# Optimization experiments

Measured on AMD Instinct MI355X. Metric: run time of the kernel, lower is better.

## Reference

```python
import jax, jax.numpy as jnp
import numpy as np

HEADS = 16
DIM_HEAD = 64
SCALE = DIM_HEAD ** -0.5

def setup_inputs() -> dict:
    key = jax.random.key(0)
    k1, k2, k3 = jax.random.split(key, 3)
    dim = HEADS * DIM_HEAD  # 1024
    x = jax.random.normal(k1, (2, 4096, dim), dtype=jnp.float32)
    w_qkv = jax.random.normal(k2, (dim, 3 * dim), dtype=jnp.float32) * (dim ** -0.5)
    w_out = jax.random.normal(k3, (dim, dim), dtype=jnp.float32) * (dim ** -0.5)
    return {"x": x, "w_qkv": w_qkv, "w_out": w_out}

def reference(x, w_qkv, w_out):
    b, n, dim = x.shape
    qkv = x @ w_qkv  # (b, n, 3*h*d)
    qkv = qkv.reshape(b, n, 3, HEADS, DIM_HEAD)
    q, k, v = (qkv[:, :, 0], qkv[:, :, 1], qkv[:, :, 2])  # (b, n, h, d)
    q = jnp.swapaxes(q, 1, 2) * SCALE  # (b, h, n, d)
    k = jnp.swapaxes(k, 1, 2)
    v = jnp.swapaxes(v, 1, 2)
    sim = jnp.einsum('bhid,bhjd->bhij', q, k)
    mask_value = -jnp.finfo(sim.dtype).max
    causal_mask = jnp.triu(jnp.ones((n, n), dtype=bool), k=1)
    sim = jnp.where(causal_mask, mask_value, sim)
    attn = jax.nn.softmax(sim, axis=-1)
    out = jnp.einsum('bhij,bhjd->bhid', attn, v)
    out = jnp.swapaxes(out, 1, 2).reshape(b, n, HEADS * DIM_HEAD)
    return out @ w_out
```

## Files before the change

kernel.cpp:

```cpp
#include <hip/hip_runtime.h>
#include <stdint.h>
#include <stddef.h>

typedef __attribute__((ext_vector_type(8))) short bf16x8;
typedef __attribute__((ext_vector_type(4))) float f32x4;
typedef __attribute__((ext_vector_type(4))) unsigned short u16x4;
typedef __attribute__((ext_vector_type(4))) unsigned int u32x4;

#define BATCH 2
#define SEQ 4096
#define NHEADS 16
#define DHEAD 64
#define DIM 1024
#define MTOT 8192
#define N1 3072
#define NEGINF -3.0e4f
#define QSCALE 0.18033688f

__device__ __forceinline__ unsigned short f2bf(float f) {
  union { float f; unsigned u; } x; x.f = f;
  unsigned r = x.u + 0x7fffu + ((x.u >> 16) & 1u);
  return (unsigned short)(r >> 16);
}

__device__ __forceinline__ float fexp2(float x) {
  return __builtin_amdgcn_exp2f(x);
}

__device__ __forceinline__ unsigned pk_bf16(float a, float b) {
  unsigned d;
  asm("v_cvt_pk_bf16_f32 %0, %1, %2" : "=v"(d) : "v"(a), "v"(b));
  return d;
}

__device__ __forceinline__ void gload_lds16(const void* g, void* l) {
  __builtin_amdgcn_global_load_lds(
      (const __attribute__((address_space(1))) void*)g,
      (__attribute__((address_space(3))) void*)l, 16, 0, 0);
}

__global__ __launch_bounds__(256) void cvt_f2b(const float* __restrict__ in,
                                               unsigned short* __restrict__ out,
                                               int n4) {
  int i = blockIdx.x * 256 + threadIdx.x;
  if (i < n4) {
    f32x4 v = ((const f32x4*)in)[i];
    u16x4 o;
#pragma unroll
    for (int j = 0; j < 4; j++) o[j] = f2bf(v[j]);
    ((u16x4*)out)[i] = o;
  }
}

__global__ void transpose_cvt(const float* __restrict__ in,
                              unsigned short* __restrict__ out, int R, int C) {
  __shared__ unsigned short t[32][33];
  int tx = threadIdx.x, ty = threadIdx.y;
  int c0 = blockIdx.x * 32, r0 = blockIdx.y * 32;
#pragma unroll
  for (int i = 0; i < 4; i++)
    t[ty + i * 8][tx] = f2bf(in[(size_t)(r0 + ty + i * 8) * C + c0 + tx]);
  __syncthreads();
#pragma unroll
  for (int i = 0; i < 4; i++)
    out[(size_t)(c0 + ty + i * 8) * R + r0 + tx] = t[tx][ty + i * 8];
}

template <int MODE>
__global__ __launch_bounds__(256) void gemm_bt(
    const unsigned short* __restrict__ A,
    const unsigned short* __restrict__ Bt,
    unsigned short* __restrict__ O0,
    unsigned short* __restrict__ O1,
    unsigned short* __restrict__ O2,
    float* __restrict__ Of,
    int N, int K) {
  __shared__ unsigned short Asl[128][32];
  __shared__ unsigned short Bsl[128][32];
  const int tid = threadIdx.x;
  const int lane = tid & 63, wv = tid >> 6;
  const int wr = wv >> 1, wc = wv & 1;
  const int m0 = blockIdx.x * 128, n0 = blockIdx.y * 128;
  const int lrow = lane >> 2, lcol = (lane & 3) * 8;
  const int fr = lane & 15, kc8 = (lane >> 4) * 8;
  f32x4 acc[4][4] = {};
  for (int k0 = 0; k0 < K; k0 += 32) {
#pragma unroll
    for (int c = 0; c < 2; c++) {
      int r = wv * 32 + c * 16 + lrow;
      gload_lds16(&A[(size_t)(m0 + r) * K + k0 + lcol], &Asl[wv * 32 + c * 16][0]);
      gload_lds16(&Bt[(size_t)(n0 + r) * K + k0 + lcol], &Bsl[wv * 32 + c * 16][0]);
    }
    __syncthreads();
    bf16x8 af[4], bfr[4];
#pragma unroll
    for (int i = 0; i < 4; i++)
      af[i] = *(const bf16x8*)&Asl[wr * 64 + i * 16 + fr][kc8];
#pragma unroll
    for (int j = 0; j < 4; j++)
      bfr[j] = *(const bf16x8*)&Bsl[wc * 64 + j * 16 + fr][kc8];
#pragma unroll
    for (int i = 0; i < 4; i++)
#pragma unroll
      for (int j = 0; j < 4; j++)
        acc[i][j] = __builtin_amdgcn_mfma_f32_16x16x32_bf16(af[i], bfr[j], acc[i][j], 0, 0, 0);
    __syncthreads();
  }
  const int rq = (lane >> 4) * 4;
#pragma unroll
  for (int i = 0; i < 4; i++) {
#pragma unroll
    for (int j = 0; j < 4; j++) {
#pragma unroll
      for (int r = 0; r < 4; r++) {
        int row = m0 + wr * 64 + i * 16 + rq + r;
        int col = n0 + wc * 64 + j * 16 + fr;
        float v = acc[i][j][r];
        if (MODE == 0) {
          int w = col >> 10, rem = col & 1023;
          int h = rem >> 6, d = rem & 63;
          int b = row >> 12, n = row & 4095;
          size_t bh = (size_t)b * NHEADS + h;
          if (w == 0)      O0[(bh * SEQ + n) * DHEAD + d] = f2bf(v * QSCALE);
          else if (w == 1) O1[(bh * SEQ + n) * DHEAD + d] = f2bf(v);
          else             O2[(bh * DHEAD + d) * SEQ + n] = f2bf(v);
        } else {
          Of[(size_t)row * N + col] = v;
        }
      }
    }
  }
}

__device__ __forceinline__ void attn_tile3(
    int qt, const unsigned short* __restrict__ Qp,
    const unsigned short* __restrict__ Kp,
    const unsigned short* __restrict__ Vp,
    unsigned short* __restrict__ AOp,
    unsigned short* __restrict__ Kl,
    unsigned short* __restrict__ Vl,
    int lane, int wv) {
  const int fr = lane & 15, g = lane >> 4;
  const int kc8 = g * 8, rq = g * 4;
  const int sw = fr & 7;
  const int q0 = qt * 64;
  const int srl = lane >> 3;
  const int jl = lane & 7;

  bf16x8 qf0 = *(const bf16x8*)&Qp[(size_t)(q0 + wv * 16 + fr) * DHEAD + kc8];
  bf16x8 qf1 = *(const bf16x8*)&Qp[(size_t)(q0 + wv * 16 + fr) * DHEAD + 32 + kc8];

  f32x4 oacc[4] = {};
  float lrow = 0.f;

#pragma unroll
  for (int c = 0; c < 2; c++) {
    int seg = wv * 2 + c;
    int r = seg * 8 + srl;
    int j = jl ^ (r & 7);
    gload_lds16(&Kp[(size_t)r * DHEAD + j * 8], Kl + seg * 512);
    gload_lds16(&Vp[(size_t)r * SEQ + j * 8], Vl + seg * 512);
  }
  __syncthreads();

  int cur = 0;
  for (int kt = 0; kt <= qt; kt++) {
    const int ktn = (kt < qt) ? kt + 1 : qt;
    unsigned short* Kc = Kl + cur * 4096;
    unsigned short* Vc = Vl + cur * 4096;
    unsigned short* Kn = Kl + (cur ^ 1) * 4096;
    unsigned short* Vn = Vl + (cur ^ 1) * 4096;
#pragma unroll
    for (int c = 0; c < 2; c++) {
      int seg = wv * 2 + c;
      int r = seg * 8 + srl;
      int j = jl ^ (r & 7);
      gload_lds16(&Kp[(size_t)(ktn * 64 + r) * DHEAD + j * 8], Kn + seg * 512);
      gload_lds16(&Vp[(size_t)r * SEQ + ktn * 64 + j * 8], Vn + seg * 512);
    }
    f32x4 sv[4];
    __builtin_amdgcn_s_setprio(1);
#pragma unroll
    for (int cb = 0; cb < 4; cb++) {
      bf16x8 kf0 = *(const bf16x8*)&Kc[(cb * 16 + fr) * 64 + ((g ^ sw) << 3)];
      bf16x8 kf1 = *(const bf16x8*)&Kc[(cb * 16 + fr) * 64 + (((4 + g) ^ sw) << 3)];
      f32x4 z = {};
      z = __builtin_amdgcn_mfma_f32_16x16x32_bf16(kf0, qf0, z, 0, 0, 0);
      sv[cb] = __builtin_amdgcn_mfma_f32_16x16x32_bf16(kf1, qf1, z, 0, 0, 0);
    }
    __builtin_amdgcn_s_setprio(0);
    if (kt == qt) {
#pragma unroll
      for (int cb = 0; cb < 4; cb++)
#pragma unroll
        for (int r = 0; r < 4; r++)
          if (cb * 16 + rq + r > wv * 16 + fr) sv[cb][r] = NEGINF;
    }
    float p[4][4];
#pragma unroll
    for (int cb = 0; cb < 4; cb++)
#pragma unroll
      for (int r = 0; r < 4; r++)
        p[cb][r] = fexp2(sv[cb][r]);
    float t0 = (p[0][0] + p[0][1]) + (p[0][2] + p[0][3]);
    float t1 = (p[1][0] + p[1][1]) + (p[1][2] + p[1][3]);
    float t2 = (p[2][0] + p[2][1]) + (p[2][2] + p[2][3]);
    float t3 = (p[3][0] + p[3][1]) + (p[3][2] + p[3][3]);
    lrow += (t0 + t1) + (t2 + t3);
    unsigned A0 = pk_bf16(p[0][0], p[0][1]), A1 = pk_bf16(p[0][2], p[0][3]);
    unsigned B0 = pk_bf16(p[1][0], p[1][1]), B1 = pk_bf16(p[1][2], p[1][3]);
    unsigned C0 = pk_bf16(p[2][0], p[2][1]), C1 = pk_bf16(p[2][2], p[2][3]);
    unsigned D0 = pk_bf16(p[3][0], p[3][1]), D1 = pk_bf16(p[3][2], p[3][3]);
    const bool lo2 = (g < 2);
    unsigned R0 = __shfl_xor((int)(lo2 ? B0 : A0), 32, 64);
    unsigned R1 = __shfl_xor((int)(lo2 ? B1 : A1), 32, 64);
    unsigned R2 = __shfl_xor((int)(lo2 ? D0 : C0), 32, 64);
    unsigned R3 = __shfl_xor((int)(lo2 ? D1 : C1), 32, 64);
    unsigned o00 = (g == 0) ? A0 : (g == 3) ? B0 : R0;
    unsigned o01 = (g == 0) ? A1 : (g == 3) ? B1 : R1;
    unsigned o10 = (g == 0) ? C0 : (g == 3) ? D0 : R2;
    unsigned o11 = (g == 0) ? C1 : (g == 3) ? D1 : R3;
    unsigned p00 = (g == 1) ? A0 : (g == 2) ? B0 : R0;
    unsigned p01 = (g == 1) ? A1 : (g == 2) ? B1 : R1;
    unsigned p10 = (g == 1) ? C0 : (g == 2) ? D0 : R2;
    unsigned p11 = (g == 1) ? C1 : (g == 2) ? D1 : R3;
    unsigned x00 = __shfl_xor((int)p00, 16, 64);
    unsigned x01 = __shfl_xor((int)p01, 16, 64);
    unsigned x10 = __shfl_xor((int)p10, 16, 64);
    unsigned x11 = __shfl_xor((int)p11, 16, 64);
    const bool odd = (g & 1);
    u32x4 f0, f1;
    f0[0] = odd ? x00 : o00; f0[1] = odd ? x01 : o01;
    f0[2] = odd ? o00 : x00; f0[3] = odd ? o01 : x01;
    f1[0] = odd ? x10 : o10; f1[1] = odd ? x11 : o11;
    f1[2] = odd ? o10 : x10; f1[3] = odd ? o11 : x11;
    bf16x8 pa0 = *(bf16x8*)&f0;
    bf16x8 pa1 = *(bf16x8*)&f1;
    __builtin_amdgcn_s_setprio(1);
#pragma unroll
    for (int db = 0; db < 4; db++) {
      bf16x8 vf0 = *(const bf16x8*)&Vc[(db * 16 + fr) * 64 + ((g ^ sw) << 3)];
      bf16x8 vf1 = *(const bf16x8*)&Vc[(db * 16 + fr) * 64 + (((4 + g) ^ sw) << 3)];
      oacc[db] = __builtin_amdgcn_mfma_f32_16x16x32_bf16(pa0, vf0, oacc[db], 0, 0, 0);
      oacc[db] = __builtin_amdgcn_mfma_f32_16x16x32_bf16(pa1, vf1, oacc[db], 0, 0, 0);
    }
    __builtin_amdgcn_s_setprio(0);
    __syncthreads();
    cur ^= 1;
  }

  lrow += __shfl_xor(lrow, 16, 64);
  lrow += __shfl_xor(lrow, 32, 64);
  float i0 = __builtin_amdgcn_rcpf(__shfl(lrow, rq + 0, 64));
  float i1 = __builtin_amdgcn_rcpf(__shfl(lrow, rq + 1, 64));
  float i2 = __builtin_amdgcn_rcpf(__shfl(lrow, rq + 2, 64));
  float i3 = __builtin_amdgcn_rcpf(__shfl(lrow, rq + 3, 64));
#pragma unroll
  for (int db = 0; db < 4; db++) {
    int nb = q0 + wv * 16 + rq;
    int d = db * 16 + fr;
    AOp[(size_t)(nb + 0) * DIM + d] = f2bf(oacc[db][0] * i0);
    AOp[(size_t)(nb + 1) * DIM + d] = f2bf(oacc[db][1] * i1);
    AOp[(size_t)(nb + 2) * DIM + d] = f2bf(oacc[db][2] * i2);
    AOp[(size_t)(nb + 3) * DIM + d] = f2bf(oacc[db][3] * i3);
  }
}

__global__ __launch_bounds__(256, 4) void attn_causal(
    const unsigned short* __restrict__ Q,
    const unsigned short* __restrict__ Kb,
    const unsigned short* __restrict__ Vt,
    unsigned short* __restrict__ AO) {
  const int id = blockIdx.x;
  const int xcd = id & 7, t = id >> 3;
  const int pi = t & 31, bq = t >> 5;
  const int bh = xcd * 4 + bq;
  const int tid = threadIdx.x, lane = tid & 63, wv = tid >> 6;

  const unsigned short* Qp = Q + (size_t)bh * SEQ * DHEAD;
  const unsigned short* Kp = Kb + (size_t)bh * SEQ * DHEAD;
  const unsigned short* Vp = Vt + (size_t)bh * DHEAD * SEQ;
  const int b = bh >> 4, h = bh & 15;
  unsigned short* AOp = AO + (size_t)b * SEQ * DIM + h * DHEAD;

  __shared__ unsigned short Kl[2][4096];
  __shared__ unsigned short Vl[2][4096];

  attn_tile3(pi, Qp, Kp, Vp, AOp, &Kl[0][0], &Vl[0][0], lane, wv);
  attn_tile3(63 - pi, Qp, Kp, Vp, AOp, &Kl[0][0], &Vl[0][0], lane, wv);
}

extern "C" void kernel_launch(void* const* d_in, const int* in_sizes, int n_in,
                              void* d_out, int out_size, void* d_ws, size_t ws_size,
                              hipStream_t stream) {
  const float* x    = (const float*)d_in[0];
  const float* wqkv = (const float*)d_in[1];
  const float* wout = (const float*)d_in[2];
  float* out = (float*)d_out;

  unsigned short* ws = (unsigned short*)d_ws;
  unsigned short* xb = ws;
  unsigned short* ao = ws;
  unsigned short* wqkv_t = ws + (size_t)MTOT * DIM;
  unsigned short* wout_t = wqkv_t + (size_t)N1 * DIM;
  unsigned short* qb = wout_t + (size_t)DIM * DIM;
  unsigned short* kb = qb + (size_t)BATCH * NHEADS * SEQ * DHEAD;
  unsigned short* vt = kb + (size_t)BATCH * NHEADS * SEQ * DHEAD;

  int n4 = (MTOT * DIM) / 4;
  hipLaunchKernelGGL(cvt_f2b, dim3(n4 / 256), dim3(256), 0, stream, x, xb, n4);

  dim3 tb(32, 8);
  hipLaunchKernelGGL(transpose_cvt, dim3(N1 / 32, DIM / 32), tb, 0, stream,
                     wqkv, wqkv_t, DIM, N1);
  hipLaunchKernelGGL(transpose_cvt, dim3(DIM / 32, DIM / 32), tb, 0, stream,
                     wout, wout_t, DIM, DIM);

  hipLaunchKernelGGL((gemm_bt<0>), dim3(MTOT / 128, N1 / 128), dim3(256), 0, stream,
                     xb, wqkv_t, qb, kb, vt, nullptr, N1, DIM);

  hipLaunchKernelGGL(attn_causal, dim3(32 * 32), dim3(256), 0, stream,
                     qb, kb, vt, ao);

  hipLaunchKernelGGL((gemm_bt<1>), dim3(MTOT / 128, DIM / 128), dim3(256), 0, stream,
                     ao, wout_t, nullptr, nullptr, nullptr, out, DIM, DIM);
}
```

Baseline: 243.3 us.

## Process paired causal query tiles together to share K/V loads

Merges the two sequential per-block attention passes (query tile pi and 63-pi) into one loop over key tiles. Each loaded K/V tile now feeds both query tiles, with the shorter tile stopping once it reaches its diagonal. This roughly halves K/V global-to-LDS traffic and barrier count per block. In exchange it raises register pressure (two accumulator sets, two Q fragments), which may limit occupancy under launch_bounds(256,4), and the block-to-tile mapping is also reordered to alternate pi direction across heads.

Result: no change. 246.9 us (+1.5%).

```diff
diff --git a/kernel.cpp b/kernel.cpp
--- a/kernel.cpp
+++ b/kernel.cpp
@@ -132,8 +132,52 @@
   }
 }
 
-__device__ __forceinline__ void attn_tile3(
-    int qt, const unsigned short* __restrict__ Qp,
+__device__ __forceinline__ void sm_pack(const f32x4 sv[4], float& lrow, int g,
+                                        bf16x8& pa0o, bf16x8& pa1o) {
+  float p[4][4];
+#pragma unroll
+  for (int cb = 0; cb < 4; cb++)
+#pragma unroll
+    for (int r = 0; r < 4; r++)
+      p[cb][r] = fexp2(sv[cb][r]);
+  float t0 = (p[0][0] + p[0][1]) + (p[0][2] + p[0][3]);
+  float t1 = (p[1][0] + p[1][1]) + (p[1][2] + p[1][3]);
+  float t2 = (p[2][0] + p[2][1]) + (p[2][2] + p[2][3]);
+  float t3 = (p[3][0] + p[3][1]) + (p[3][2] + p[3][3]);
+  lrow += (t0 + t1) + (t2 + t3);
+  unsigned A0 = pk_bf16(p[0][0], p[0][1]), A1 = pk_bf16(p[0][2], p[0][3]);
+  unsigned B0 = pk_bf16(p[1][0], p[1][1]), B1 = pk_bf16(p[1][2], p[1][3]);
+  unsigned C0 = pk_bf16(p[2][0], p[2][1]), C1 = pk_bf16(p[2][2], p[2][3]);
+  unsigned D0 = pk_bf16(p[3][0], p[3][1]), D1 = pk_bf16(p[3][2], p[3][3]);
+  const bool lo2 = (g < 2);
+  unsigned R0 = __shfl_xor((int)(lo2 ? B0 : A0), 32, 64);
+  unsigned R1 = __shfl_xor((int)(lo2 ? B1 : A1), 32, 64);
+  unsigned R2 = __shfl_xor((int)(lo2 ? D0 : C0), 32, 64);
+  unsigned R3 = __shfl_xor((int)(lo2 ? D1 : C1), 32, 64);
+  unsigned o00 = (g == 0) ? A0 : (g == 3) ? B0 : R0;
+  unsigned o01 = (g == 0) ? A1 : (g == 3) ? B1 : R1;
+  unsigned o10 = (g == 0) ? C0 : (g == 3) ? D0 : R2;
+  unsigned o11 = (g == 0) ? C1 : (g == 3) ? D1 : R3;
+  unsigned p00 = (g == 1) ? A0 : (g == 2) ? B0 : R0;
+  unsigned p01 = (g == 1) ? A1 : (g == 2) ? B1 : R1;
+  unsigned p10 = (g == 1) ? C0 : (g == 2) ? D0 : R2;
+  unsigned p11 = (g == 1) ? C1 : (g == 2) ? D1 : R3;
+  unsigned x00 = __shfl_xor((int)p00, 16, 64);
+  unsigned x01 = __shfl_xor((int)p01, 16, 64);
+  unsigned x10 = __shfl_xor((int)p10, 16, 64);
+  unsigned x11 = __shfl_xor((int)p11, 16, 64);
+  const bool odd = (g & 1);
+  u32x4 f0, f1;
+  f0[0] = odd ? x00 : o00; f0[1] = odd ? x01 : o01;
+  f0[2] = odd ? o00 : x00; f0[3] = odd ? o01 : x01;
+  f1[0] = odd ? x10 : o10; f1[1] = odd ? x11 : o11;
+  f1[2] = odd ? o10 : x10; f1[3] = odd ? o11 : x11;
+  pa0o = *(bf16x8*)&f0;
+  pa1o = *(bf16x8*)&f1;
+}
+
+__device__ __forceinline__ void attn_dual(
+    int ta, int tb, const unsigned short* __restrict__ Qp,
     const unsigned short* __restrict__ Kp,
     const unsigned short* __restrict__ Vp,
     unsigned short* __restrict__ AOp,
@@ -143,15 +187,17 @@
   const int fr = lane & 15, g = lane >> 4;
   const int kc8 = g * 8, rq = g * 4;
   const int sw = fr & 7;
-  const int q0 = qt * 64;
+  const int q0A = ta * 64, q0B = tb * 64;
   const int srl = lane >> 3;
   const int jl = lane & 7;
 
-  bf16x8 qf0 = *(const bf16x8*)&Qp[(size_t)(q0 + wv * 16 + fr) * DHEAD + kc8];
-  bf16x8 qf1 = *(const bf16x8*)&Qp[(size_t)(q0 + wv * 16 + fr) * DHEAD + 32 + kc8];
-
-  f32x4 oacc[4] = {};
-  float lrow = 0.f;
+  bf16x8 qA0 = *(const bf16x8*)&Qp[(size_t)(q0A + wv * 16 + fr) * DHEAD + kc8];
+  bf16x8 qA1 = *(const bf16x8*)&Qp[(size_t)(q0A + wv * 16 + fr) * DHEAD + 32 + kc8];
+  bf16x8 qB0 = *(const bf16x8*)&Qp[(size_t)(q0B + wv * 16 + fr) * DHEAD + kc8];
+  bf16x8 qB1 = *(const bf16x8*)&Qp[(size_t)(q0B + wv * 16 + fr) * DHEAD + 32 + kc8];
+
+  f32x4 oA[4] = {}, oB[4] = {};
+  float lA = 0.f, lB = 0.f;
 
 #pragma unroll
   for (int c = 0; c < 2; c++) {
@@ -164,8 +210,9 @@
   __syncthreads();
 
   int cur = 0;
-  for (int kt = 0; kt <= qt; kt++) {
-    const int ktn = (kt < qt) ? kt + 1 : qt;
+  for (int kt = 0; kt <= tb; kt++) {
+    const int ktn = (kt < tb) ? kt + 1 : tb;
+    const bool doA = (kt <= ta);
     unsigned short* Kc = Kl + cur * 4096;
     unsigned short* Vc = Vl + cur * 4096;
     unsigned short* Kn = Kl + (cur ^ 1) * 4096;
@@ -178,91 +225,76 @@
       gload_lds16(&Kp[(size_t)(ktn * 64 + r) * DHEAD + j * 8], Kn + seg * 512);
       gload_lds16(&Vp[(size_t)r * SEQ + ktn * 64 + j * 8], Vn + seg * 512);
     }
-    f32x4 sv[4];
+    f32x4 svA[4], svB[4];
     __builtin_amdgcn_s_setprio(1);
 #pragma unroll
     for (int cb = 0; cb < 4; cb++) {
       bf16x8 kf0 = *(const bf16x8*)&Kc[(cb * 16 + fr) * 64 + ((g ^ sw) << 3)];
       bf16x8 kf1 = *(const bf16x8*)&Kc[(cb * 16 + fr) * 64 + (((4 + g) ^ sw) << 3)];
-      f32x4 z = {};
-      z = __builtin_amdgcn_mfma_f32_16x16x32_bf16(kf0, qf0, z, 0, 0, 0);
-      sv[cb] = __builtin_amdgcn_mfma_f32_16x16x32_bf16(kf1, qf1, z, 0, 0, 0);
+      f32x4 zb = {};
+      zb = __builtin_amdgcn_mfma_f32_16x16x32_bf16(kf0, qB0, zb, 0, 0, 0);
+      svB[cb] = __builtin_amdgcn_mfma_f32_16x16x32_bf16(kf1, qB1, zb, 0, 0, 0);
+      if (doA) {
+        f32x4 za = {};
+        za = __builtin_amdgcn_mfma_f32_16x16x32_bf16(kf0, qA0, za, 0, 0, 0);
+        svA[cb] = __builtin_amdgcn_mfma_f32_16x16x32_bf16(kf1, qA1, za, 0, 0, 0);
+      }
     }
     __builtin_amdgcn_s_setprio(0);
-    if (kt == qt) {
+    if (kt == ta) {
 #pragma unroll
       for (int cb = 0; cb < 4; cb++)
 #pragma unroll
         for (int r = 0; r < 4; r++)
-          if (cb * 16 + rq + r > wv * 16 + fr) sv[cb][r] = NEGINF;
-    }
-    float p[4][4];
-#pragma unroll
-    for (int cb = 0; cb < 4; cb++)
-#pragma unroll
-      for (int r = 0; r < 4; r++)
-        p[cb][r] = fexp2(sv[cb][r]);
-    float t0 = (p[0][0] + p[0][1]) + (p[0][2] + p[0][3]);
-    float t1 = (p[1][0] + p[1][1]) + (p[1][2] + p[1][3]);
-    float t2 = (p[2][0] + p[2][1]) + (p[2][2] + p[2][3]);
-    float t3 = (p[3][0] + p[3][1]) + (p[3][2] + p[3][3]);
-    lrow += (t0 + t1) + (t2 + t3);
-    unsigned A0 = pk_bf16(p[0][0], p[0][1]), A1 = pk_bf16(p[0][2], p[0][3]);
-    unsigned B0 = pk_bf16(p[1][0], p[1][1]), B1 = pk_bf16(p[1][2], p[1][3]);
-    unsigned C0 = pk_bf16(p[2][0], p[2][1]), C1 = pk_bf16(p[2][2], p[2][3]);
-    unsigned D0 = pk_bf16(p[3][0], p[3][1]), D1 = pk_bf16(p[3][2], p[3][3]);
-    const bool lo2 = (g < 2);
-    unsigned R0 = __shfl_xor((int)(lo2 ? B0 : A0), 32, 64);
-    unsigned R1 = __shfl_xor((int)(lo2 ? B1 : A1), 32, 64);
-    unsigned R2 = __shfl_xor((int)(lo2 ? D0 : C0), 32, 64);
-    unsigned R3 = __shfl_xor((int)(lo2 ? D1 : C1), 32, 64);
-    unsigned o00 = (g == 0) ? A0 : (g == 3) ? B0 : R0;
-    unsigned o01 = (g == 0) ? A1 : (g == 3) ? B1 : R1;
-    unsigned o10 = (g == 0) ? C0 : (g == 3) ? D0 : R2;
-    unsigned o11 = (g == 0) ? C1 : (g == 3) ? D1 : R3;
-    unsigned p00 = (g == 1) ? A0 : (g == 2) ? B0 : R0;
-    unsigned p01 = (g == 1) ? A1 : (g == 2) ? B1 : R1;
-    unsigned p10 = (g == 1) ? C0 : (g == 2) ? D0 : R2;
-    unsigned p11 = (g == 1) ? C1 : (g == 2) ? D1 : R3;
-    unsigned x00 = __shfl_xor((int)p00, 16, 64);
-    unsigned x01 = __shfl_xor((int)p01, 16, 64);
-    unsigned x10 = __shfl_xor((int)p10, 16, 64);
-    unsigned x11 = __shfl_xor((int)p11, 16, 64);
-    const bool odd = (g & 1);
-    u32x4 f0, f1;
-    f0[0] = odd ? x00 : o00; f0[1] = odd ? x01 : o01;
-    f0[2] = odd ? o00 : x00; f0[3] = odd ? o01 : x01;
-    f1[0] = odd ? x10 : o10; f1[1] = odd ? x11 : o11;
-    f1[2] = odd ? o10 : x10; f1[3] = odd ? o11 : x11;
-    bf16x8 pa0 = *(bf16x8*)&f0;
-    bf16x8 pa1 = *(bf16x8*)&f1;
+          if (cb * 16 + rq + r > wv * 16 + fr) svA[cb][r] = NEGINF;
+    }
+    if (kt == tb) {
+#pragma unroll
+      for (int cb = 0; cb < 4; cb++)
+#pragma unroll
+        for (int r = 0; r < 4; r++)
+          if (cb * 16 + rq + r > wv * 16 + fr) svB[cb][r] = NEGINF;
+    }
+    bf16x8 paA0 = {}, paA1 = {}, paB0, paB1;
+    if (doA) sm_pack(svA, lA, g, paA0, paA1);
+    sm_pack(svB, lB, g, paB0, paB1);
     __builtin_amdgcn_s_setprio(1);
 #pragma unroll
     for (int db = 0; db < 4; db++) {
       bf16x8 vf0 = *(const bf16x8*)&Vc[(db * 16 + fr) * 64 + ((g ^ sw) << 3)];
       bf16x8 vf1 = *(const bf16x8*)&Vc[(db * 16 + fr) * 64 + (((4 + g) ^ sw) << 3)];
-      oacc[db] = __builtin_amdgcn_mfma_f32_16x16x32_bf16(pa0, vf0, oacc[db], 0, 0, 0);
-      oacc[db] = __builtin_amdgcn_mfma_f32_16x16x32_bf16(pa1, vf1, oacc[db], 0, 0, 0);
+      oB[db] = __builtin_amdgcn_mfma_f32_16x16x32_bf16(paB0, vf0, oB[db], 0, 0, 0);
+      oB[db] = __builtin_amdgcn_mfma_f32_16x16x32_bf16(paB1, vf1, oB[db], 0, 0, 0);
+      if (doA) {
+        oA[db] = __builtin_amdgcn_mfma_f32_16x16x32_bf16(paA0, vf0, oA[db], 0, 0, 0);
+        oA[db] = __builtin_amdgcn_mfma_f32_16x16x32_bf16(paA1, vf1, oA[db], 0, 0, 0);
+      }
     }
     __builtin_amdgcn_s_setprio(0);
     __syncthreads();
     cur ^= 1;
   }
 
-  lrow += __shfl_xor(lrow, 16, 64);
-  lrow += __shfl_xor(lrow, 32, 64);
-  float i0 = __builtin_amdgcn_rcpf(__shfl(lrow, rq + 0, 64));
-  float i1 = __builtin_amdgcn_rcpf(__shfl(lrow, rq + 1, 64));
-  float i2 = __builtin_amdgcn_rcpf(__shfl(lrow, rq + 2, 64));
-  float i3 = __builtin_amdgcn_rcpf(__shfl(lrow, rq + 3, 64));
-#pragma unroll
-  for (int db = 0; db < 4; db++) {
-    int nb = q0 + wv * 16 + rq;
-    int d = db * 16 + fr;
-    AOp[(size_t)(nb + 0) * DIM + d] = f2bf(oacc[db][0] * i0);
-    AOp[(size_t)(nb + 1) * DIM + d] = f2bf(oacc[db][1] * i1);
-    AOp[(size_t)(nb + 2) * DIM + d] = f2bf(oacc[db][2] * i2);
-    AOp[(size_t)(nb + 3) * DIM + d] = f2bf(oacc[db][3] * i3);
+#pragma unroll
+  for (int s = 0; s < 2; s++) {
+    float lrow = s ? lB : lA;
+    const f32x4* oacc = s ? oB : oA;
+    int q0 = s ? q0B : q0A;
+    lrow += __shfl_xor(lrow, 16, 64);
+    lrow += __shfl_xor(lrow, 32, 64);
+    float i0 = __builtin_amdgcn_rcpf(__shfl(lrow, rq + 0, 64));
+    float i1 = __builtin_amdgcn_rcpf(__shfl(lrow, rq + 1, 64));
+    float i2 = __builtin_amdgcn_rcpf(__shfl(lrow, rq + 2, 64));
+    float i3 = __builtin_amdgcn_rcpf(__shfl(lrow, rq + 3, 64));
+#pragma unroll
+    for (int db = 0; db < 4; db++) {
+      int nb = q0 + wv * 16 + rq;
+      int d = db * 16 + fr;
+      AOp[(size_t)(nb + 0) * DIM + d] = f2bf(oacc[db][0] * i0);
+      AOp[(size_t)(nb + 1) * DIM + d] = f2bf(oacc[db][1] * i1);
+      AOp[(size_t)(nb + 2) * DIM + d] = f2bf(oacc[db][2] * i2);
+      AOp[(size_t)(nb + 3) * DIM + d] = f2bf(oacc[db][3] * i3);
+    }
   }
 }
 
@@ -272,9 +304,12 @@
     const unsigned short* __restrict__ Vt,
     unsigned short* __restrict__ AO) {
   const int id = blockIdx.x;
-  const int xcd = id & 7, t = id >> 3;
-  const int pi = t & 31, bq = t >> 5;
-  const int bh = xcd * 4 + bq;
+  const int xcd = id & 7;
+  const int inner = id >> 3;
+  const int c = inner & 31;
+  const int k = inner >> 5;
+  const int pi = (k & 1) ? (31 - c) : c;
+  const int bh = xcd * 4 + k;
   const int tid = threadIdx.x, lane = tid & 63, wv = tid >> 6;
 
   const unsigned short* Qp = Q + (size_t)bh * SEQ * DHEAD;
@@ -286,8 +321,7 @@
   __shared__ unsigned short Kl[2][4096];
   __shared__ unsigned short Vl[2][4096];
 
-  attn_tile3(pi, Qp, Kp, Vp, AOp, &Kl[0][0], &Vl[0][0], lane, wv);
-  attn_tile3(63 - pi, Qp, Kp, Vp, AOp, &Kl[0][0], &Vl[0][0], lane, wv);
+  attn_dual(pi, 63 - pi, Qp, Kp, Vp, AOp, &Kl[0][0], &Vl[0][0], lane, wv);
 }
 
 extern "C" void kernel_launch(void* const* d_in, const int* in_sizes, int n_in,
@@ -319,7 +353,7 @@
   hipLaunchKernelGGL((gemm_bt<0>), dim3(MTOT / 128, N1 / 128), dim3(256), 0, stream,
                      xb, wqkv_t, qb, kb, vt, nullptr, N1, DIM);
 
-  hipLaunchKernelGGL(attn_causal, dim3(32 * 32), dim3(256), 0, stream,
+  hipLaunchKernelGGL(attn_causal, dim3(1024), dim3(256), 0, stream,
                      qb, kb, vt, ao);
 
   hipLaunchKernelGGL((gemm_bt<1>), dim3(MTOT / 128, DIM / 128), dim3(256), 0, stream,
```
